# Kernel optimization log

Measured on AMD Instinct MI355X. Metric: run time of the kernel, lower is better.

Reference implementation:

```python
import jax, jax.numpy as jnp
import numpy as np

B, S, D = 4, 2048, 1024  # batch, seq_len, d_model == d_internal


def setup_inputs() -> dict:
    key = jax.random.key(0)
    ks = jax.random.split(key, 7)
    s = 1.0 / np.sqrt(D)  # scale weights so softmax / relu stay in a sane range
    return {
        "input_vecs": jax.random.normal(ks[0], (B, S, D), jnp.float32),
        "Wq": jax.random.normal(ks[1], (D, D), jnp.float32) * s,
        "Wk": jax.random.normal(ks[2], (D, D), jnp.float32) * s,
        "Wv": jax.random.normal(ks[3], (D, D), jnp.float32) * s,
        "W1": jax.random.normal(ks[4], (D, D), jnp.float32) * s,  # linear1: d_internal -> d_model
        "b1": jnp.zeros((D,), jnp.float32),
        "W2": jax.random.normal(ks[5], (D, D), jnp.float32) * s,  # linear2: d_model -> d_internal
        "b2": jnp.zeros((D,), jnp.float32),
    }


def reference(input_vecs, Wq, Wk, Wv, W1, b1, W2, b2):
    d_internal = Wq.shape[1]
    # single-head self-attention: Q,K,V = X @ Wq/Wk/Wv
    q = jnp.einsum("bsd,de->bse", input_vecs, Wq)
    k = jnp.einsum("bsd,de->bse", input_vecs, Wk)
    v = jnp.einsum("bsd,de->bse", input_vecs, Wv)
    scores = jnp.einsum("bqe,bke->bqk", q, k) / jnp.sqrt(jnp.asarray(d_internal, q.dtype))
    attn = jax.nn.softmax(scores, axis=-1)               # [B, S, S]
    attn_out = jnp.einsum("bqk,bke->bqe", attn, v)       # [B, S, D]
    h = attn_out + input_vecs                            # residual 1
    h = jax.nn.relu(h @ W1 + b1)                         # linear1 + relu
    out = h @ W2 + b2 + input_vecs                       # linear2 + residual 2
    return out, attn
```

## Files before the change

### kernel.cpp

```cpp
#include <hip/hip_runtime.h>
#include <hip/hip_bf16.h>

typedef unsigned short u16;
typedef unsigned int   u32;
typedef u16   u16x8 __attribute__((ext_vector_type(8)));
typedef u16   u16x4 __attribute__((ext_vector_type(4)));
typedef __bf16 bf16x8 __attribute__((ext_vector_type(8)));
typedef float f32x4 __attribute__((ext_vector_type(4)));

__device__ __forceinline__ u16 f2bf(float f) {
    u32 u = __float_as_uint(f);
    u = u + 0x7FFFu + ((u >> 16) & 1u);
    return (u16)(u >> 16);
}

__device__ __forceinline__ void gload16(const u16* g, u16* l) {
    __builtin_amdgcn_global_load_lds(
        (const __attribute__((address_space(1))) void*)g,
        (__attribute__((address_space(3))) void*)l,
        16, 0, 0);
}

#define WAITV(N) asm volatile("s_waitcnt vmcnt(" #N ")" ::: "memory")
#define SCHEDB() __builtin_amdgcn_sched_barrier(0)
#define BAR()    __builtin_amdgcn_s_barrier()

__global__ __launch_bounds__(256) void cvt_x(const float* __restrict__ X,
                                             u16* __restrict__ Xb) {
    const long i = (long)(blockIdx.x * 256 + threadIdx.x) * 8;
    float4 a = *(const float4*)(X + i);
    float4 b = *(const float4*)(X + i + 4);
    u16x8 r;
    r[0] = f2bf(a.x); r[1] = f2bf(a.y); r[2] = f2bf(a.z); r[3] = f2bf(a.w);
    r[4] = f2bf(b.x); r[5] = f2bf(b.y); r[6] = f2bf(b.z); r[7] = f2bf(b.w);
    *(u16x8*)(Xb + i) = r;
}

__global__ __launch_bounds__(256) void cvt_wT(const float* __restrict__ w0,
                                              const float* __restrict__ w1,
                                              const float* __restrict__ w2,
                                              const float* __restrict__ w3,
                                              const float* __restrict__ w4,
                                              u16* __restrict__ wt) {
    const float* srcs[5] = {w0, w1, w2, w3, w4};
    const float* W = srcs[blockIdx.z];
    u16* WT = wt + (long)blockIdx.z * 1048576;
    __shared__ float t[32][33];
    const int tx = threadIdx.x, ty = threadIdx.y;
    const int n0 = blockIdx.x * 32, k0 = blockIdx.y * 32;
    #pragma unroll
    for (int r = 0; r < 4; ++r)
        t[ty + 8 * r][tx] = W[(long)(k0 + ty + 8 * r) * 1024 + n0 + tx];
    __syncthreads();
    #pragma unroll
    for (int r = 0; r < 4; ++r)
        WT[(long)(n0 + ty + 8 * r) * 1024 + k0 + tx] = f2bf(t[tx][ty + 8 * r]);
}

enum { EPI_QKV = 0, EPI_SCALE_F32 = 2, EPI_ADDX_BF16 = 3,
       EPI_BIAS_RELU_BF16 = 4, EPI_BIAS_ADDX_F32 = 5 };

#define BM3 256
#define BN3 128
#define BK3 32
#define S3_A (BM3 * BK3)
#define S3_B (BN3 * BK3)
#define S3SZ (S3_A + S3_B)

template <int EPI>
__global__ __launch_bounds__(512, 2)
void gemm_bt32(const u16* __restrict__ A, const u16* __restrict__ Bt,
               void* __restrict__ Cout, void* __restrict__ CoutK,
               void* __restrict__ CoutV,
               const int M, const int N, const int K,
               const long sA, const long sB,
               const float scale) {
    const int GX = gridDim.x, GY = gridDim.y;
    const int p  = blockIdx.x + GX * (blockIdx.y + GY * blockIdx.z);
    const int slab = (p & 7) + 8 * (p / (8 * GY));
    const int vy   = (p >> 3) % GY;
    const int vx   = slab % GX;
    const int bz   = slab / GX;

    const u16* Ab = A + (long)bz * sA;
    const u16* Bb = Bt + (long)bz * sB;

    const int tid  = threadIdx.x;
    const int lane = tid & 63;
    const int w    = tid >> 6;
    const int wrg  = (w >> 1) * 64;
    const int wcg  = (w & 1) * 64;
    const int m0   = vx * BM3;
    const int n0   = vy * BN3;

    __shared__ __align__(16) u16 LDS[3 * S3SZ];

    f32x4 acc[4][4] = {};

    const long Kl = K;
    const int schunk = ((lane & 3) ^ ((lane >> 3) & 3)) * 8;
    const u16* Ag = Ab + (long)(m0 + w * 32 + (lane >> 2)) * Kl + schunk;
    const u16* Bg = Bb + (long)(n0 + w * 16 + (lane >> 2)) * Kl + schunk;

    const int rbase = lane & 15;
    const int koff  = ((lane >> 4) ^ ((rbase >> 1) & 3)) * 8;

    const int dAoff = (w * 32) * BK3;
    const int dBoff = S3_A + (w * 16) * BK3;

    #define LDA3(mi) (*(const bf16x8*)(Asl + (wrg + (mi) * 16 + rbase) * BK3 + koff))
    #define LDB3(ni) (*(const bf16x8*)(Bsl + (wcg + (ni) * 16 + rbase) * BK3 + koff))
    #define STAGE3(KT, SLOT) do {                                  \
        u16* a_ = &LDS[(SLOT) * S3SZ + dAoff];                     \
        u16* b_ = &LDS[(SLOT) * S3SZ + dBoff];                     \
        gload16(Ag + (KT), a_);                                    \
        gload16(Ag + (KT) + 16 * Kl, a_ + 16 * BK3);               \
        gload16(Bg + (KT), b_);                                    \
    } while (0)

    const int nt = K / BK3;
    STAGE3(0, 0);
    STAGE3(BK3, 1);
    WAITV(3);
    BAR();

    int s = 0;
    for (int t = 0; t < nt; ++t) {
        const u16* Asl = &LDS[s * S3SZ];
        const u16* Bsl = &LDS[s * S3SZ + S3_A];
        const int s2 = (s + 2 >= 3) ? s - 1 : s + 2;
        const bool st = (t + 2 < nt);

        if (st) STAGE3((long)(t + 2) * BK3, s2);

        bf16x8 af[4], bf[4];
        #pragma unroll
        for (int mi = 0; mi < 4; ++mi) af[mi] = LDA3(mi);
        #pragma unroll
        for (int ni = 0; ni < 4; ++ni) bf[ni] = LDB3(ni);
        #pragma unroll
        for (int mi = 0; mi < 4; ++mi)
            #pragma unroll
            for (int ni = 0; ni < 4; ++ni)
                acc[mi][ni] = __builtin_amdgcn_mfma_f32_16x16x32_bf16(
                    af[mi], bf[ni], acc[mi][ni], 0, 0, 0);

        SCHEDB();
        if (st) { WAITV(3); } else { WAITV(0); }
        BAR();
        SCHEDB();
        s = (s == 2) ? 0 : s + 1;
    }
    #undef LDA3
    #undef LDB3
    #undef STAGE3

    const int colb = wcg + (lane & 15);
    const int rq   = (lane >> 4) * 4;
    #pragma unroll
    for (int mi = 0; mi < 4; ++mi) {
        #pragma unroll
        for (int ni = 0; ni < 4; ++ni) {
            f32x4 v = acc[mi][ni];
            const int gr0 = m0 + wrg + mi * 16 + rq;
            const int gc  = n0 + colb + ni * 16;
            if (bz == 2) {
                u16x4 p2;
                p2[0] = f2bf(v[0]); p2[1] = f2bf(v[1]);
                p2[2] = f2bf(v[2]); p2[3] = f2bf(v[3]);
                u16* C = (u16*)CoutV;
                const long off = ((long)(gr0 >> 11)) * 2097152 +
                                 (long)gc * 2048 + (gr0 & 2047);
                *(u16x4*)(C + off) = p2;
            } else {
                u16* C = (u16*)(bz == 0 ? Cout : CoutK);
                #pragma unroll
                for (int j = 0; j < 4; ++j)
                    C[(long)(gr0 + j) * N + gc] = f2bf(v[j]);
            }
        }
    }
}

#define BM 256
#define BN 128
#define BKW 64
#define SLOT_A (BM * BKW)
#define SLOT_B (BN * BKW)
#define SLOTSZ (SLOT_A + SLOT_B)

template <int EPI>
__global__ __launch_bounds__(512, 1)
void gemm_bt(const u16* __restrict__ A, const u16* __restrict__ Bt,
             void* __restrict__ Cout,
             const float* __restrict__ bias, const float* __restrict__ Xres,
             const int M, const int N, const int K,
             const long sA, const long sB, const long sC, const long sX,
             const float scale) {
    const int GX = gridDim.x, GY = gridDim.y;
    const int p  = blockIdx.x + GX * (blockIdx.y + GY * blockIdx.z);
    const int slab = (p & 7) + 8 * (p / (8 * GY));
    const int vy   = (p >> 3) % GY;
    const int vx   = slab % GX;
    const int bz   = slab / GX;

    const u16* Ab = A + (long)bz * sA;
    const u16* Bb = Bt + (long)bz * sB;
    const float* Xr = Xres ? Xres + (long)bz * sX : nullptr;

    const int tid  = threadIdx.x;
    const int lane = tid & 63;
    const int w    = tid >> 6;
    const int wrg  = (w >> 1) * 64;
    const int wcg  = (w & 1) * 64;
    const int m0   = vx * BM;
    const int n0   = vy * BN;

    __shared__ __align__(16) u16 LDS[3 * SLOTSZ];

    f32x4 acc[4][4] = {};

    const long Kl = K;
    const int schunk = ((lane & 7) ^ (lane >> 3)) * 8;
    const u16* Ag = Ab + (long)(m0 + w * 32 + (lane >> 3)) * Kl + schunk;
    const u16* Bg = Bb + (long)(n0 + w * 16 + (lane >> 3)) * Kl + schunk;

    const int rbase = lane & 15;
    const int rx    = rbase & 7;
    const int q4    = lane >> 4;

    const int dAoff = (w * 32) * BKW;
    const int dBoff = SLOT_A + (w * 16) * BKW;

    #define LDA(mi, ks) (*(const bf16x8*)(Asl + (wrg + (mi) * 16 + rbase) * BKW \
                         + ((((ks) * 4 + q4) ^ rx)) * 8))
    #define LDB(ni, ks) (*(const bf16x8*)(Bsl + (wcg + (ni) * 16 + rbase) * BKW \
                         + ((((ks) * 4 + q4) ^ rx)) * 8))

    const int nt = K / BKW;
    {
        u16* d0 = &LDS[0];
        gload16(Ag, d0 + dAoff);
        gload16(Ag + 8 * Kl,  d0 + dAoff + 512);
        gload16(Ag + 16 * Kl, d0 + dAoff + 1024);
        gload16(Ag + 24 * Kl, d0 + dAoff + 1536);
        gload16(Bg, d0 + dBoff);
        gload16(Bg + 8 * Kl,  d0 + dBoff + 512);
        u16* d1 = &LDS[SLOTSZ];
        gload16(Ag + BKW, d1 + dAoff);
        gload16(Ag + BKW + 8 * Kl,  d1 + dAoff + 512);
        gload16(Ag + BKW + 16 * Kl, d1 + dAoff + 1024);
        gload16(Ag + BKW + 24 * Kl, d1 + dAoff + 1536);
        gload16(Bg + BKW, d1 + dBoff);
        gload16(Bg + BKW + 8 * Kl,  d1 + dBoff + 512);
    }
    WAITV(6);
    BAR();

    int s = 0;
    for (int t = 0; t < nt; ++t) {
        const u16* Asl = &LDS[s * SLOTSZ];
        const u16* Bsl = &LDS[s * SLOTSZ + SLOT_A];
        const int s2 = (s + 2 >= 3) ? s - 1 : s + 2;
        u16* dA = &LDS[s2 * SLOTSZ] + dAoff;
        u16* dB = &LDS[s2 * SLOTSZ] + dBoff;
        const bool st = (t + 2 < nt);
        const long kt2 = (long)(t + 2) * BKW;

        if (st) {
            gload16(Ag + kt2, dA);
            gload16(Ag + kt2 + 8 * Kl,  dA + 512);
            gload16(Ag + kt2 + 16 * Kl, dA + 1024);
            gload16(Ag + kt2 + 24 * Kl, dA + 1536);
            gload16(Bg + kt2, dB);
            gload16(Bg + kt2 + 8 * Kl,  dB + 512);
        }

        bf16x8 af[4][2], bf[4][2];
        #pragma unroll
        for (int mi = 0; mi < 4; ++mi) {
            af[mi][0] = LDA(mi, 0);
            af[mi][1] = LDA(mi, 1);
        }
        #pragma unroll
        for (int ni = 0; ni < 4; ++ni) {
            bf[ni][0] = LDB(ni, 0);
            bf[ni][1] = LDB(ni, 1);
        }
        #pragma unroll
        for (int ks = 0; ks < 2; ++ks)
            #pragma unroll
            for (int mi = 0; mi < 4; ++mi)
                #pragma unroll
                for (int ni = 0; ni < 4; ++ni)
                    acc[mi][ni] = __builtin_amdgcn_mfma_f32_16x16x32_bf16(
                        af[mi][ks], bf[ni][ks], acc[mi][ni], 0, 0, 0);

        SCHEDB();
        if (st) { WAITV(6); } else { WAITV(0); }
        BAR();
        SCHEDB();
        s = (s == 2) ? 0 : s + 1;
    }
    #undef LDA
    #undef LDB

    const int colb = wcg + (lane & 15);
    const int rq   = (lane >> 4) * 4;
    #pragma unroll
    for (int mi = 0; mi < 4; ++mi) {
        #pragma unroll
        for (int ni = 0; ni < 4; ++ni) {
            f32x4 v = acc[mi][ni];
            const int gr0 = m0 + wrg + mi * 16 + rq;
            const int gc  = n0 + colb + ni * 16;
            #pragma unroll
            for (int j = 0; j < 4; ++j) {
                const long idx = (long)(gr0 + j) * N + gc;
                float val = v[j];
                if constexpr (EPI == EPI_ADDX_BF16) {
                    val += Xr[idx];
                    ((u16*)Cout + (long)bz * sC)[idx] = f2bf(val);
                } else if constexpr (EPI == EPI_BIAS_RELU_BF16) {
                    val = fmaxf(val + bias[gc], 0.0f);
                    ((u16*)Cout + (long)bz * sC)[idx] = f2bf(val);
                } else if constexpr (EPI == EPI_BIAS_ADDX_F32) {
                    ((float*)Cout + (long)bz * sC)[idx] =
                        val + bias[gc] + Xr[idx];
                }
            }
        }
    }
}

#define GBM 256
#define GBN 256
#define GBK 64
#define GSLOT_A (GBM * GBK)
#define GSLOTSZ (2 * GSLOT_A)

template <int EPI>
__global__ __launch_bounds__(512, 1)
void gemm_big(const u16* __restrict__ A, const u16* __restrict__ Bt,
              void* __restrict__ Cout,
              const int N, const int K,
              const long sA, const long sB, const long sC,
              const float scale) {
    const int GX = gridDim.x, GY = gridDim.y;
    const int p  = blockIdx.x + GX * (blockIdx.y + GY * blockIdx.z);
    const int slab = (p & 7) + 8 * (p / (8 * GY));
    const int vy   = (p >> 3) % GY;
    const int vx   = slab % GX;
    const int bz   = slab / GX;

    const u16* Ab = A + (long)bz * sA;
    const u16* Bb = Bt + (long)bz * sB;

    const int tid  = threadIdx.x;
    const int lane = tid & 63;
    const int w    = tid >> 6;
    const int wrg  = (w >> 2) * 128;
    const int wcg  = (w & 3) * 64;
    const int m0   = vx * GBM;
    const int n0   = vy * GBN;

    __shared__ __align__(16) u16 LDS[2 * GSLOTSZ];

    f32x4 acc[8][4] = {};

    const long Kl = K;
    const int schunk = ((lane & 7) ^ (lane >> 3)) * 8;
    const u16* Ag = Ab + (long)(m0 + w * 32 + (lane >> 3)) * Kl + schunk;
    const u16* Bg = Bb + (long)(n0 + w * 32 + (lane >> 3)) * Kl + schunk;

    const int rbase = lane & 15;
    const int rx    = rbase & 7;
    const int q4    = lane >> 4;

    const int dAoff = (w * 32) * GBK;
    const int dBoff = GSLOT_A + (w * 32) * GBK;

    #define GLDA(mi, ks) (*(const bf16x8*)(Asl + (wrg + (mi) * 16 + rbase) * GBK \
                          + ((((ks) * 4 + q4) ^ rx)) * 8))
    #define GLDB(ni, ks) (*(const bf16x8*)(Bsl + (wcg + (ni) * 16 + rbase) * GBK \
                          + ((((ks) * 4 + q4) ^ rx)) * 8))
    #define GSTAGE_A(KT, D) do {                       \
        gload16(Ag + (KT), (D));                       \
        gload16(Ag + (KT) + 8 * Kl,  (D) + 512);       \
        gload16(Ag + (KT) + 16 * Kl, (D) + 1024);      \
        gload16(Ag + (KT) + 24 * Kl, (D) + 1536);      \
    } while (0)
    #define GSTAGE_B(KT, D) do {                       \
        gload16(Bg + (KT), (D));                       \
        gload16(Bg + (KT) + 8 * Kl,  (D) + 512);       \
        gload16(Bg + (KT) + 16 * Kl, (D) + 1024);      \
        gload16(Bg + (KT) + 24 * Kl, (D) + 1536);      \
    } while (0)

    const int nt = K / GBK;
    GSTAGE_A(0, &LDS[0] + dAoff);
    GSTAGE_B(0, &LDS[0] + dBoff);
    WAITV(0);
    BAR();

    for (int t = 0; t < nt; ++t) {
        const int s = t & 1;
        const u16* Asl = &LDS[s * GSLOTSZ];
        const u16* Bsl = &LDS[s * GSLOTSZ] + GSLOT_A;
        u16* dnx = &LDS[(s ^ 1) * GSLOTSZ];
        const bool st = (t + 1 < nt);
        const long kt1 = (long)(t + 1) * GBK;

        if (st) {
            GSTAGE_A(kt1, dnx + dAoff);
            GSTAGE_B(kt1, dnx + dBoff);
        }

        bf16x8 bf[4][2];
        #pragma unroll
        for (int ni = 0; ni < 4; ++ni) {
            bf[ni][0] = GLDB(ni, 0);
            bf[ni][1] = GLDB(ni, 1);
        }
        bf16x8 a0 = GLDA(0, 0), a1 = GLDA(0, 1);
        #pragma unroll
        for (int mi = 0; mi < 8; ++mi) {
            bf16x8 c0 = a0, c1 = a1;
            if (mi < 7) { a0 = GLDA(mi + 1, 0); a1 = GLDA(mi + 1, 1); }
            #pragma unroll
            for (int ni = 0; ni < 4; ++ni) {
                acc[mi][ni] = __builtin_amdgcn_mfma_f32_16x16x32_bf16(
                    c0, bf[ni][0], acc[mi][ni], 0, 0, 0);
                acc[mi][ni] = __builtin_amdgcn_mfma_f32_16x16x32_bf16(
                    c1, bf[ni][1], acc[mi][ni], 0, 0, 0);
            }
        }

        SCHEDB();
        WAITV(0);
        BAR();
        SCHEDB();
    }
    #undef GLDA
    #undef GLDB
    #undef GSTAGE_A
    #undef GSTAGE_B

    const int colb = wcg + (lane & 15);
    const int rq   = (lane >> 4) * 4;
    #pragma unroll
    for (int mi = 0; mi < 8; ++mi) {
        #pragma unroll
        for (int ni = 0; ni < 4; ++ni) {
            f32x4 v = acc[mi][ni];
            const int gr0 = m0 + wrg + mi * 16 + rq;
            const int gc  = n0 + colb + ni * 16;
            if constexpr (EPI == EPI_SCALE_F32) {
                float* C = (float*)Cout + (long)bz * sC;
                #pragma unroll
                for (int j = 0; j < 4; ++j)
                    C[(long)(gr0 + j) * N + gc] = v[j] * scale;
            }
        }
    }
}

__global__ __launch_bounds__(256)
void softmax_rows(float* __restrict__ attn, u16* __restrict__ P) {
    const int row  = blockIdx.x;
    float* rp      = attn + (long)row * 2048;
    const int tid  = threadIdx.x;
    const int lane = tid & 63;
    const int w    = tid >> 6;

    float4 v0 = *(const float4*)(rp + tid * 8);
    float4 v1 = *(const float4*)(rp + tid * 8 + 4);

    float m = fmaxf(fmaxf(fmaxf(v0.x, v0.y), fmaxf(v0.z, v0.w)),
                    fmaxf(fmaxf(v1.x, v1.y), fmaxf(v1.z, v1.w)));
    #pragma unroll
    for (int o = 32; o > 0; o >>= 1) m = fmaxf(m, __shfl_xor(m, o));
    __shared__ float redm[4];
    if (lane == 0) redm[w] = m;
    __syncthreads();
    m = fmaxf(fmaxf(redm[0], redm[1]), fmaxf(redm[2], redm[3]));

    float e[8];
    e[0] = __expf(v0.x - m); e[1] = __expf(v0.y - m);
    e[2] = __expf(v0.z - m); e[3] = __expf(v0.w - m);
    e[4] = __expf(v1.x - m); e[5] = __expf(v1.y - m);
    e[6] = __expf(v1.z - m); e[7] = __expf(v1.w - m);
    float s = ((e[0] + e[1]) + (e[2] + e[3])) + ((e[4] + e[5]) + (e[6] + e[7]));
    #pragma unroll
    for (int o = 32; o > 0; o >>= 1) s += __shfl_xor(s, o);
    __shared__ float reds[4];
    if (lane == 0) reds[w] = s;
    __syncthreads();
    s = (reds[0] + reds[1]) + (reds[2] + reds[3]);
    const float inv = 1.0f / s;

    float4 o0, o1;
    o0.x = e[0] * inv; o0.y = e[1] * inv; o0.z = e[2] * inv; o0.w = e[3] * inv;
    o1.x = e[4] * inv; o1.y = e[5] * inv; o1.z = e[6] * inv; o1.w = e[7] * inv;
    *(float4*)(rp + tid * 8)     = o0;
    *(float4*)(rp + tid * 8 + 4) = o1;

    u16x8 pb;
    pb[0] = f2bf(o0.x); pb[1] = f2bf(o0.y); pb[2] = f2bf(o0.z); pb[3] = f2bf(o0.w);
    pb[4] = f2bf(o1.x); pb[5] = f2bf(o1.y); pb[6] = f2bf(o1.z); pb[7] = f2bf(o1.w);
    *(u16x8*)(P + (long)row * 2048 + tid * 8) = pb;
}

extern "C" void kernel_launch(void* const* d_in, const int* in_sizes, int n_in,
                              void* d_out, int out_size, void* d_ws, size_t ws_size,
                              hipStream_t stream) {
    const float* X  = (const float*)d_in[0];
    const float* Wq = (const float*)d_in[1];
    const float* Wk = (const float*)d_in[2];
    const float* Wv = (const float*)d_in[3];
    const float* W1 = (const float*)d_in[4];
    const float* b1 = (const float*)d_in[5];
    const float* W2 = (const float*)d_in[6];
    const float* b2 = (const float*)d_in[7];

    float* out  = (float*)d_out;
    float* attn = out + (size_t)8388608;

    char* ws = (char*)d_ws;
    u16* Xb  = (u16*)(ws);
    u16* Qb  = (u16*)(ws + (size_t)16 * 1024 * 1024);
    u16* Kb  = (u16*)(ws + (size_t)32 * 1024 * 1024);
    u16* VT  = (u16*)(ws + (size_t)48 * 1024 * 1024);
    u16* H1b = (u16*)(ws + (size_t)64 * 1024 * 1024);
    u16* WTs = (u16*)(ws + (size_t)80 * 1024 * 1024);
    u16* W1T = WTs + (size_t)3 * 1048576;
    u16* W2T = WTs + (size_t)4 * 1048576;
    u16* Pb  = Xb;
    u16* Hb  = Kb;

    cvt_x<<<4096, 256, 0, stream>>>(X, Xb);
    cvt_wT<<<dim3(32, 32, 5), dim3(32, 8), 0, stream>>>(Wq, Wk, Wv, W1, W2, WTs);

    gemm_bt32<EPI_QKV><<<dim3(32, 8, 3), 512, 0, stream>>>(
        Xb, WTs, Qb, Kb, VT, 8192, 1024, 1024, 0, 1048576, 1.0f);

    gemm_big<EPI_SCALE_F32><<<dim3(8, 8, 4), 512, 0, stream>>>(
        Qb, Kb, attn, 2048, 1024,
        2048L * 1024, 2048L * 1024, 2048L * 2048, 0.03125f);

    softmax_rows<<<8192, 256, 0, stream>>>(attn, Pb);

    gemm_bt<EPI_ADDX_BF16><<<dim3(8, 8, 4), 512, 0, stream>>>(
        Pb, VT, Hb, nullptr, X, 2048, 1024, 2048,
        2048L * 2048, 1024L * 2048, 2048L * 1024, 2048L * 1024, 1.0f);

    gemm_bt<EPI_BIAS_RELU_BF16><<<dim3(32, 8, 1), 512, 0, stream>>>(
        Hb, W1T, H1b, b1, nullptr, 8192, 1024, 1024, 0, 0, 0, 0, 1.0f);

    gemm_bt<EPI_BIAS_ADDX_F32><<<dim3(32, 8, 1), 512, 0, stream>>>(
        H1b, W2T, out, b2, X, 8192, 1024, 1024, 0, 0, 0, 0, 1.0f);
}
```

Baseline: 237.3 us.

## Retile score and PV GEMMs with smaller tiles for higher occupancy

Result: slower. 244.7 us (+3.1%).

```diff
diff --git a/kernel.cpp b/kernel.cpp
--- a/kernel.cpp
+++ b/kernel.cpp
@@ -73,7 +73,7 @@
                void* __restrict__ Cout, void* __restrict__ CoutK,
                void* __restrict__ CoutV,
                const int M, const int N, const int K,
-               const long sA, const long sB,
+               const long sA, const long sB, const long sC,
                const float scale) {
     const int GX = gridDim.x, GY = gridDim.y;
     const int p  = blockIdx.x + GX * (blockIdx.y + GY * blockIdx.z);
@@ -164,34 +164,40 @@
             f32x4 v = acc[mi][ni];
             const int gr0 = m0 + wrg + mi * 16 + rq;
             const int gc  = n0 + colb + ni * 16;
-            if (bz == 2) {
-                u16x4 p2;
-                p2[0] = f2bf(v[0]); p2[1] = f2bf(v[1]);
-                p2[2] = f2bf(v[2]); p2[3] = f2bf(v[3]);
-                u16* C = (u16*)CoutV;
-                const long off = ((long)(gr0 >> 11)) * 2097152 +
-                                 (long)gc * 2048 + (gr0 & 2047);
-                *(u16x4*)(C + off) = p2;
-            } else {
-                u16* C = (u16*)(bz == 0 ? Cout : CoutK);
+            if constexpr (EPI == EPI_QKV) {
+                if (bz == 2) {
+                    u16x4 p2;
+                    p2[0] = f2bf(v[0]); p2[1] = f2bf(v[1]);
+                    p2[2] = f2bf(v[2]); p2[3] = f2bf(v[3]);
+                    u16* C = (u16*)CoutV;
+                    const long off = ((long)(gr0 >> 11)) * 2097152 +
+                                     (long)gc * 2048 + (gr0 & 2047);
+                    *(u16x4*)(C + off) = p2;
+                } else {
+                    u16* C = (u16*)(bz == 0 ? Cout : CoutK);
+                    #pragma unroll
+                    for (int j = 0; j < 4; ++j)
+                        C[(long)(gr0 + j) * N + gc] = f2bf(v[j]);
+                }
+            } else if constexpr (EPI == EPI_SCALE_F32) {
+                float* C = (float*)Cout + (long)bz * sC;
                 #pragma unroll
                 for (int j = 0; j < 4; ++j)
-                    C[(long)(gr0 + j) * N + gc] = f2bf(v[j]);
+                    C[(long)(gr0 + j) * N + gc] = v[j] * scale;
             }
         }
     }
 }
 
-#define BM 256
+#define BM 128
 #define BN 128
-#define BKW 64
-#define SLOT_A (BM * BKW)
-#define SLOT_B (BN * BKW)
-#define SLOTSZ (SLOT_A + SLOT_B)
+#define BK 32
+#define SLOT_A (BM * BK)
+#define SLOTSZ (2 * SLOT_A)
 
 template <int EPI>
-__global__ __launch_bounds__(512, 1)
-void gemm_bt(const u16* __restrict__ A, const u16* __restrict__ Bt,
+__global__ __launch_bounds__(256, 3)
+void gemm128(const u16* __restrict__ A, const u16* __restrict__ Bt,
              void* __restrict__ Cout,
              const float* __restrict__ bias, const float* __restrict__ Xres,
              const int M, const int N, const int K,
@@ -221,40 +227,31 @@
     f32x4 acc[4][4] = {};
 
     const long Kl = K;
-    const int schunk = ((lane & 7) ^ (lane >> 3)) * 8;
-    const u16* Ag = Ab + (long)(m0 + w * 32 + (lane >> 3)) * Kl + schunk;
-    const u16* Bg = Bb + (long)(n0 + w * 16 + (lane >> 3)) * Kl + schunk;
+    const int schunk = ((lane & 3) ^ ((lane >> 3) & 3)) * 8;
+    const u16* Ag = Ab + (long)(m0 + w * 32 + (lane >> 2)) * Kl + schunk;
+    const u16* Bg = Bb + (long)(n0 + w * 32 + (lane >> 2)) * Kl + schunk;
 
     const int rbase = lane & 15;
-    const int rx    = rbase & 7;
-    const int q4    = lane >> 4;
-
-    const int dAoff = (w * 32) * BKW;
-    const int dBoff = SLOT_A + (w * 16) * BKW;
-
-    #define LDA(mi, ks) (*(const bf16x8*)(Asl + (wrg + (mi) * 16 + rbase) * BKW \
-                         + ((((ks) * 4 + q4) ^ rx)) * 8))
-    #define LDB(ni, ks) (*(const bf16x8*)(Bsl + (wcg + (ni) * 16 + rbase) * BKW \
-                         + ((((ks) * 4 + q4) ^ rx)) * 8))
-
-    const int nt = K / BKW;
-    {
-        u16* d0 = &LDS[0];
-        gload16(Ag, d0 + dAoff);
-        gload16(Ag + 8 * Kl,  d0 + dAoff + 512);
-        gload16(Ag + 16 * Kl, d0 + dAoff + 1024);
-        gload16(Ag + 24 * Kl, d0 + dAoff + 1536);
-        gload16(Bg, d0 + dBoff);
-        gload16(Bg + 8 * Kl,  d0 + dBoff + 512);
-        u16* d1 = &LDS[SLOTSZ];
-        gload16(Ag + BKW, d1 + dAoff);
-        gload16(Ag + BKW + 8 * Kl,  d1 + dAoff + 512);
-        gload16(Ag + BKW + 16 * Kl, d1 + dAoff + 1024);
-        gload16(Ag + BKW + 24 * Kl, d1 + dAoff + 1536);
-        gload16(Bg + BKW, d1 + dBoff);
-        gload16(Bg + BKW + 8 * Kl,  d1 + dBoff + 512);
-    }
-    WAITV(6);
+    const int koff  = ((lane >> 4) ^ ((rbase >> 1) & 3)) * 8;
+
+    const int dAoff = (w * 32) * BK;
+    const int dBoff = SLOT_A + (w * 32) * BK;
+
+    #define LDA(mi) (*(const bf16x8*)(Asl + (wrg + (mi) * 16 + rbase) * BK + koff))
+    #define LDB(ni) (*(const bf16x8*)(Bsl + (wcg + (ni) * 16 + rbase) * BK + koff))
+    #define STAGE(KT, SLOT) do {                                   \
+        u16* a_ = &LDS[(SLOT) * SLOTSZ + dAoff];                   \
+        u16* b_ = &LDS[(SLOT) * SLOTSZ + dBoff];                   \
+        gload16(Ag + (KT), a_);                                    \
+        gload16(Ag + (KT) + 16 * Kl, a_ + 512);                    \
+        gload16(Bg + (KT), b_);                                    \
+        gload16(Bg + (KT) + 16 * Kl, b_ + 512);                    \
+    } while (0)
+
+    const int nt = K / BK;
+    STAGE(0, 0);
+    STAGE(BK, 1);
+    WAITV(4);
     BAR();
 
     int s = 0;
@@ -262,48 +259,31 @@
         const u16* Asl = &LDS[s * SLOTSZ];
         const u16* Bsl = &LDS[s * SLOTSZ + SLOT_A];
         const int s2 = (s + 2 >= 3) ? s - 1 : s + 2;
-        u16* dA = &LDS[s2 * SLOTSZ] + dAoff;
-        u16* dB = &LDS[s2 * SLOTSZ] + dBoff;
         const bool st = (t + 2 < nt);
-        const long kt2 = (long)(t + 2) * BKW;
-
-        if (st) {
-            gload16(Ag + kt2, dA);
-            gload16(Ag + kt2 + 8 * Kl,  dA + 512);
-            gload16(Ag + kt2 + 16 * Kl, dA + 1024);
-            gload16(Ag + kt2 + 24 * Kl, dA + 1536);
-            gload16(Bg + kt2, dB);
-            gload16(Bg + kt2 + 8 * Kl,  dB + 512);
-        }
-
-        bf16x8 af[4][2], bf[4][2];
-        #pragma unroll
-        for (int mi = 0; mi < 4; ++mi) {
-            af[mi][0] = LDA(mi, 0);
-            af[mi][1] = LDA(mi, 1);
-        }
-        #pragma unroll
-        for (int ni = 0; ni < 4; ++ni) {
-            bf[ni][0] = LDB(ni, 0);
-            bf[ni][1] = LDB(ni, 1);
-        }
-        #pragma unroll
-        for (int ks = 0; ks < 2; ++ks)
+
+        if (st) STAGE((long)(t + 2) * BK, s2);
+
+        bf16x8 af[4], bf[4];
+        #pragma unroll
+        for (int mi = 0; mi < 4; ++mi) af[mi] = LDA(mi);
+        #pragma unroll
+        for (int ni = 0; ni < 4; ++ni) bf[ni] = LDB(ni);
+        #pragma unroll
+        for (int mi = 0; mi < 4; ++mi)
             #pragma unroll
-            for (int mi = 0; mi < 4; ++mi)
-                #pragma unroll
-                for (int ni = 0; ni < 4; ++ni)
-                    acc[mi][ni] = __builtin_amdgcn_mfma_f32_16x16x32_bf16(
-                        af[mi][ks], bf[ni][ks], acc[mi][ni], 0, 0, 0);
+            for (int ni = 0; ni < 4; ++ni)
+                acc[mi][ni] = __builtin_amdgcn_mfma_f32_16x16x32_bf16(
+                    af[mi], bf[ni], acc[mi][ni], 0, 0, 0);
 
         SCHEDB();
-        if (st) { WAITV(6); } else { WAITV(0); }
+        if (st) { WAITV(4); } else { WAITV(0); }
         BAR();
         SCHEDB();
         s = (s == 2) ? 0 : s + 1;
     }
     #undef LDA
     #undef LDB
+    #undef STAGE
 
     const int colb = wcg + (lane & 15);
     const int rq   = (lane >> 4) * 4;
@@ -333,19 +313,21 @@
     }
 }
 
-#define GBM 256
-#define GBN 256
-#define GBK 64
-#define GSLOT_A (GBM * GBK)
-#define GSLOTSZ (2 * GSLOT_A)
+#define BML 256
+#define BNL 128
+#define BKW 64
+#define LSLOT_A (BML * BKW)
+#define LSLOT_B (BNL * BKW)
+#define LSLOTSZ (LSLOT_A + LSLOT_B)
 
 template <int EPI>
 __global__ __launch_bounds__(512, 1)
-void gemm_big(const u16* __restrict__ A, const u16* __restrict__ Bt,
-              void* __restrict__ Cout,
-              const int N, const int K,
-              const long sA, const long sB, const long sC,
-              const float scale) {
+void gemm_bt(const u16* __restrict__ A, const u16* __restrict__ Bt,
+             void* __restrict__ Cout,
+             const float* __restrict__ bias, const float* __restrict__ Xres,
+             const int M, const int N, const int K,
+             const long sA, const long sB, const long sC, const long sX,
+             const float scale) {
     const int GX = gridDim.x, GY = gridDim.y;
     const int p  = blockIdx.x + GX * (blockIdx.y + GY * blockIdx.z);
     const int slab = (p & 7) + 8 * (p / (8 * GY));
@@ -355,111 +337,128 @@
 
     const u16* Ab = A + (long)bz * sA;
     const u16* Bb = Bt + (long)bz * sB;
+    const float* Xr = Xres ? Xres + (long)bz * sX : nullptr;
 
     const int tid  = threadIdx.x;
     const int lane = tid & 63;
     const int w    = tid >> 6;
-    const int wrg  = (w >> 2) * 128;
-    const int wcg  = (w & 3) * 64;
-    const int m0   = vx * GBM;
-    const int n0   = vy * GBN;
-
-    __shared__ __align__(16) u16 LDS[2 * GSLOTSZ];
-
-    f32x4 acc[8][4] = {};
+    const int wrg  = (w >> 1) * 64;
+    const int wcg  = (w & 1) * 64;
+    const int m0   = vx * BML;
+    const int n0   = vy * BNL;
+
+    __shared__ __align__(16) u16 LDS[3 * LSLOTSZ];
+
+    f32x4 acc[4][4] = {};
 
     const long Kl = K;
     const int schunk = ((lane & 7) ^ (lane >> 3)) * 8;
     const u16* Ag = Ab + (long)(m0 + w * 32 + (lane >> 3)) * Kl + schunk;
-    const u16* Bg = Bb + (long)(n0 + w * 32 + (lane >> 3)) * Kl + schunk;
+    const u16* Bg = Bb + (long)(n0 + w * 16 + (lane >> 3)) * Kl + schunk;
 
     const int rbase = lane & 15;
     const int rx    = rbase & 7;
     const int q4    = lane >> 4;
 
-    const int dAoff = (w * 32) * GBK;
-    const int dBoff = GSLOT_A + (w * 32) * GBK;
-
-    #define GLDA(mi, ks) (*(const bf16x8*)(Asl + (wrg + (mi) * 16 + rbase) * GBK \
-                          + ((((ks) * 4 + q4) ^ rx)) * 8))
-    #define GLDB(ni, ks) (*(const bf16x8*)(Bsl + (wcg + (ni) * 16 + rbase) * GBK \
-                          + ((((ks) * 4 + q4) ^ rx)) * 8))
-    #define GSTAGE_A(KT, D) do {                       \
-        gload16(Ag + (KT), (D));                       \
-        gload16(Ag + (KT) + 8 * Kl,  (D) + 512);       \
-        gload16(Ag + (KT) + 16 * Kl, (D) + 1024);      \
-        gload16(Ag + (KT) + 24 * Kl, (D) + 1536);      \
-    } while (0)
-    #define GSTAGE_B(KT, D) do {                       \
-        gload16(Bg + (KT), (D));                       \
-        gload16(Bg + (KT) + 8 * Kl,  (D) + 512);       \
-        gload16(Bg + (KT) + 16 * Kl, (D) + 1024);      \
-        gload16(Bg + (KT) + 24 * Kl, (D) + 1536);      \
-    } while (0)
-
-    const int nt = K / GBK;
-    GSTAGE_A(0, &LDS[0] + dAoff);
-    GSTAGE_B(0, &LDS[0] + dBoff);
-    WAITV(0);
+    const int dAoff = (w * 32) * BKW;
+    const int dBoff = LSLOT_A + (w * 16) * BKW;
+
+    #define LDAL(mi, ks) (*(const bf16x8*)(Asl + (wrg + (mi) * 16 + rbase) * BKW \
+                         + ((((ks) * 4 + q4) ^ rx)) * 8))
+    #define LDBL(ni, ks) (*(const bf16x8*)(Bsl + (wcg + (ni) * 16 + rbase) * BKW \
+                         + ((((ks) * 4 + q4) ^ rx)) * 8))
+
+    const int nt = K / BKW;
+    {
+        u16* d0 = &LDS[0];
+        gload16(Ag, d0 + dAoff);
+        gload16(Ag + 8 * Kl,  d0 + dAoff + 512);
+        gload16(Ag + 16 * Kl, d0 + dAoff + 1024);
+        gload16(Ag + 24 * Kl, d0 + dAoff + 1536);
+        gload16(Bg, d0 + dBoff);
+        gload16(Bg + 8 * Kl,  d0 + dBoff + 512);
+        u16* d1 = &LDS[LSLOTSZ];
+        gload16(Ag + BKW, d1 + dAoff);
+        gload16(Ag + BKW + 8 * Kl,  d1 + dAoff + 512);
+        gload16(Ag + BKW + 16 * Kl, d1 + dAoff + 1024);
+        gload16(Ag + BKW + 24 * Kl, d1 + dAoff + 1536);
+        gload16(Bg + BKW, d1 + dBoff);
+        gload16(Bg + BKW + 8 * Kl,  d1 + dBoff + 512);
+    }
+    WAITV(6);
     BAR();
 
+    int s = 0;
     for (int t = 0; t < nt; ++t) {
-        const int s = t & 1;
-        const u16* Asl = &LDS[s * GSLOTSZ];
-        const u16* Bsl = &LDS[s * GSLOTSZ] + GSLOT_A;
-        u16* dnx = &LDS[(s ^ 1) * GSLOTSZ];
-        const bool st = (t + 1 < nt);
-        const long kt1 = (long)(t + 1) * GBK;
+        const u16* Asl = &LDS[s * LSLOTSZ];
+        const u16* Bsl = &LDS[s * LSLOTSZ + LSLOT_A];
+        const int s2 = (s + 2 >= 3) ? s - 1 : s + 2;
+        u16* dA = &LDS[s2 * LSLOTSZ] + dAoff;
+        u16* dB = &LDS[s2 * LSLOTSZ] + dBoff;
+        const bool st = (t + 2 < nt);
+        const long kt2 = (long)(t + 2) * BKW;
 
         if (st) {
-            GSTAGE_A(kt1, dnx + dAoff);
-            GSTAGE_B(kt1, dnx + dBoff);
+            gload16(Ag + kt2, dA);
+            gload16(Ag + kt2 + 8 * Kl,  dA + 512);
+            gload16(Ag + kt2 + 16 * Kl, dA + 1024);
+            gload16(Ag + kt2 + 24 * Kl, dA + 1536);
+            gload16(Bg + kt2, dB);
+            gload16(Bg + kt2 + 8 * Kl,  dB + 512);
         }
 
-        bf16x8 bf[4][2];
+        bf16x8 af[4][2], bf[4][2];
+        #pragma unroll
+        for (int mi = 0; mi < 4; ++mi) {
+            af[mi][0] = LDAL(mi, 0);
+            af[mi][1] = LDAL(mi, 1);
+        }
         #pragma unroll
         for (int ni = 0; ni < 4; ++ni) {
-            bf[ni][0] = GLDB(ni, 0);
-            bf[ni][1] = GLDB(ni, 1);
+            bf[ni][0] = LDBL(ni, 0);
+            bf[ni][1] = LDBL(ni, 1);
         }
-        bf16x8 a0 = GLDA(0, 0), a1 = GLDA(0, 1);
-        #pragma unroll
-        for (int mi = 0; mi < 8; ++mi) {
-            bf16x8 c0 = a0, c1 = a1;
-            if (mi < 7) { a0 = GLDA(mi + 1, 0); a1 = GLDA(mi + 1, 1); }
+        #pragma unroll
+        for (int ks = 0; ks < 2; ++ks)
             #pragma unroll
-            for (int ni = 0; ni < 4; ++ni) {
-                acc[mi][ni] = __builtin_amdgcn_mfma_f32_16x16x32_bf16(
-                    c0, bf[ni][0], acc[mi][ni], 0, 0, 0);
-                acc[mi][ni] = __builtin_amdgcn_mfma_f32_16x16x32_bf16(
-                    c1, bf[ni][1], acc[mi][ni], 0, 0, 0);
-            }
-        }
+            for (int mi = 0; mi < 4; ++mi)
+                #pragma unroll
+                for (int ni = 0; ni < 4; ++ni)
+                    acc[mi][ni] = __builtin_amdgcn_mfma_f32_16x16x32_bf16(
+                        af[mi][ks], bf[ni][ks], acc[mi][ni], 0, 0, 0);
 
         SCHEDB();
-        WAITV(0);
+        if (st) { WAITV(6); } else { WAITV(0); }
         BAR();
         SCHEDB();
-    }
-    #undef GLDA
-    #undef GLDB
-    #undef GSTAGE_A
-    #undef GSTAGE_B
+        s = (s == 2) ? 0 : s + 1;
+    }
+    #undef LDAL
+    #undef LDBL
 
     const int colb = wcg + (lane & 15);
     const int rq   = (lane >> 4) * 4;
     #pragma unroll
-    for (int mi = 0; mi < 8; ++mi) {
+    for (int mi = 0; mi < 4; ++mi) {
         #pragma unroll
         for (int ni = 0; ni < 4; ++ni) {
             f32x4 v = acc[mi][ni];
             const int gr0 = m0 + wrg + mi * 16 + rq;
             const int gc  = n0 + colb + ni * 16;
-            if constexpr (EPI == EPI_SCALE_F32) {
-                float* C = (float*)Cout + (long)bz * sC;
-                #pragma unroll
-                for (int j = 0; j < 4; ++j)
-                    C[(long)(gr0 + j) * N + gc] = v[j] * scale;
+            #pragma unroll
+            for (int j = 0; j < 4; ++j) {
+                const long idx = (long)(gr0 + j) * N + gc;
+                float val = v[j];
+                if constexpr (EPI == EPI_ADDX_BF16) {
+                    val += Xr[idx];
+                    ((u16*)Cout + (long)bz * sC)[idx] = f2bf(val);
+                } else if constexpr (EPI == EPI_BIAS_RELU_BF16) {
+                    val = fmaxf(val + bias[gc], 0.0f);
+                    ((u16*)Cout + (long)bz * sC)[idx] = f2bf(val);
+                } else if constexpr (EPI == EPI_BIAS_ADDX_F32) {
+                    ((float*)Cout + (long)bz * sC)[idx] =
+                        val + bias[gc] + Xr[idx];
+                }
             }
         }
     }
@@ -542,15 +541,15 @@
     cvt_wT<<<dim3(32, 32, 5), dim3(32, 8), 0, stream>>>(Wq, Wk, Wv, W1, W2, WTs);
 
     gemm_bt32<EPI_QKV><<<dim3(32, 8, 3), 512, 0, stream>>>(
-        Xb, WTs, Qb, Kb, VT, 8192, 1024, 1024, 0, 1048576, 1.0f);
-
-    gemm_big<EPI_SCALE_F32><<<dim3(8, 8, 4), 512, 0, stream>>>(
-        Qb, Kb, attn, 2048, 1024,
+        Xb, WTs, Qb, Kb, VT, 8192, 1024, 1024, 0, 1048576, 0, 1.0f);
+
+    gemm_bt32<EPI_SCALE_F32><<<dim3(8, 16, 4), 512, 0, stream>>>(
+        Qb, Kb, attn, nullptr, nullptr, 2048, 2048, 1024,
         2048L * 1024, 2048L * 1024, 2048L * 2048, 0.03125f);
 
     softmax_rows<<<8192, 256, 0, stream>>>(attn, Pb);
 
-    gemm_bt<EPI_ADDX_BF16><<<dim3(8, 8, 4), 512, 0, stream>>>(
+    gemm128<EPI_ADDX_BF16><<<dim3(16, 8, 4), 256, 0, stream>>>(
         Pb, VT, Hb, nullptr, X, 2048, 1024, 2048,
         2048L * 2048, 1024L * 2048, 2048L * 1024, 2048L * 1024, 1.0f);
 
```
